# Optimization experiments

Measured on AMD Instinct MI355X. Metric: run time of the kernel, lower is better.

Reference implementation:

```python
import jax, jax.numpy as jnp
import numpy as np

BILATERAL = True
THETA_ALPHA = 8.0   # spatial bandwidth for bilateral term
THETA_BETA = 0.5    # color bandwidth for bilateral term
THETA_GAMMA = 3.0   # spatial bandwidth for spatial-only term


def _features(input_image):
    # input_image: [B, Ci, H, W] -> features [B, N, D]
    B, Ci, H, W = input_image.shape
    N = H * W
    ys, xs = jnp.meshgrid(jnp.arange(H, dtype=jnp.float32),
                          jnp.arange(W, dtype=jnp.float32), indexing='ij')
    pos = jnp.stack([ys, xs], axis=-1).reshape(N, 2)  # [N, 2]
    if BILATERAL:
        sp = jnp.broadcast_to(pos / THETA_ALPHA, (B, N, 2))
        col = input_image.reshape(B, Ci, N).transpose(0, 2, 1) / THETA_BETA  # [B, N, Ci]
        return jnp.concatenate([sp, col], axis=-1)  # [B, N, 2+Ci]
    else:
        return jnp.broadcast_to(pos / THETA_GAMMA, (B, N, 2))


def _gauss_filter(values, feats):
    # values: [B, C, N]; feats: [B, N, D] -> [B, C, N]
    # K_ij = exp(-0.5 * ||f_i - f_j||^2) (unnormalized, as in permutohedral filtering)
    sq = jnp.sum(feats * feats, axis=-1)  # [B, N]
    # squared distances: [B, N, N]
    d2 = sq[:, :, None] + sq[:, None, :] - 2.0 * jnp.einsum('bnd,bmd->bnm', feats, feats)
    K = jnp.exp(-0.5 * jnp.maximum(d2, 0.0))
    return jnp.einsum('bnm,bcm->bcn', K, values)


def setup_inputs() -> dict:
    key = jax.random.key(0)
    k1, k2 = jax.random.split(key)
    cur_state = jax.random.normal(k1, (2, 21, 96, 96), dtype=jnp.float32)
    input_image = jax.random.uniform(k2, (2, 3, 96, 96), dtype=jnp.float32)
    return {"cur_state": cur_state, "input_image": input_image}


def reference(cur_state, input_image):
    assert cur_state.ndim == 4
    B, C, H, W = cur_state.shape
    N = H * W
    feats = _features(input_image)                 # [B, N, D]
    vals = cur_state.reshape(B, C, N)              # [B, C, N]
    out = _gauss_filter(vals, feats)               # [B, C, N]
    return out.reshape(B, C, H, W)
```

## Files before the change

### kernel.cpp

```cpp
#include <hip/hip_runtime.h>
#include <hip/hip_bf16.h>
#include <math.h>


#define HH 96
#define WW 96
#define NN (HH * WW)
#define NB 2
#define NC 21

typedef __attribute__((ext_vector_type(8))) short short8;
typedef __attribute__((ext_vector_type(16))) float f32x16;
typedef __attribute__((ext_vector_type(2))) float float2v;

constexpr float INV_TA = 0.125f;
constexpr float INV_TB = 2.0f;
constexpr float LOG2E  = 1.44269504088896340736f;

constexpr int BLK    = 256;
constexpr int ITILE  = 64;
constexpr int NIT    = NN / ITILE;
constexpr int G      = 12;
constexpr int NPIECE = 36;
constexpr int NP     = NPIECE / G;

constexpr size_t VG_BYTES = (size_t)NB * NPIECE * 1024 * 16;
constexpr size_t FJA_OFF  = VG_BYTES;

constexpr int SMEM_BYTES = 4 * 32 * 33 * 4;

constexpr int NVU  = NB * NPIECE * 1024;
constexpr int NFT  = NB * NN;
constexpr int PREP_TASKS = NVU + NFT;

#if defined(__has_builtin)
#if __has_builtin(__builtin_amdgcn_exp2f)
#define EXP2F(x) __builtin_amdgcn_exp2f(x)
#endif
#if __has_builtin(__builtin_amdgcn_cvt_pk_bf16_f32)
#define HAS_CVT_PK_BF16 1
#endif
#endif
#ifndef EXP2F
#define EXP2F(x) exp2f(x)
#endif

__device__ __forceinline__ unsigned short bfh(float f) {
    return (unsigned short)((__float_as_uint(f) + 0x8000u) >> 16);
}
__device__ __forceinline__ float bff(unsigned short u) {
    return __uint_as_float(((unsigned)u) << 16);
}
__device__ __forceinline__ unsigned pack2bf(float a, float b) {
#ifdef HAS_CVT_PK_BF16
    auto t = __builtin_amdgcn_cvt_pk_bf16_f32(a, b);
    unsigned r; __builtin_memcpy(&r, &t, 4); return r;
#else
    const unsigned u0 = __float_as_uint(a) + 0x8000u;
    const unsigned u1 = __float_as_uint(b) + 0x8000u;
    return __builtin_amdgcn_perm(u1, u0, 0x07060302u);
#endif
}

__global__ __launch_bounds__(BLK)
void prep_kernel(const float* __restrict__ cur, const float* __restrict__ img,
                 unsigned char* __restrict__ ws) {
    const int t = blockIdx.x * BLK + threadIdx.x;
    if (t < NVU) {
        const int b  = t / (NPIECE * 1024);
        const int r  = t % (NPIECE * 1024);
        const int rr = r & 1023;
        const int piece = r >> 10;
        const int jbl = rr >> 7;
        const int m   = (rr >> 6) & 1;
        const int h   = (rr >> 5) & 1;
        const int c   = rr & 31;
        const int jb = piece * 256 + jbl * 32 + m * 16 + 4 * h;
        float4 qa = {0, 0, 0, 0}, qb = {0, 0, 0, 0};
        if (c < NC) {
            const float* row = cur + ((size_t)b * NC + c) * NN;
            qa = *(const float4*)(row + jb);
            qb = *(const float4*)(row + jb + 8);
        }
        uint4 o;
        o.x = pack2bf(qa.x, qa.y); o.y = pack2bf(qa.z, qa.w);
        o.z = pack2bf(qb.x, qb.y); o.w = pack2bf(qb.z, qb.w);
        *(uint4*)(ws + (size_t)t * 16) = o;
    } else {
        const int tf = t - NVU;
        const int b = tf / NN;
        const int j = tf % NN;
        const float y = (float)(j / WW) * INV_TA;
        const float x = (float)(j % WW) * INV_TA;
        const float* ib = img + (size_t)b * 3 * NN;
        unsigned short ch[3], cl[3]; float cf[3];
        #pragma unroll
        for (int d = 0; d < 3; ++d) {
            const float c = ib[d * NN + j] * INV_TB;
            ch[d] = bfh(c);
            const float chf = bff(ch[d]);
            cl[d] = bfh(c - chf);
            cf[d] = chf + bff(cl[d]);
        }
        const float e = -0.5f * (y * y + x * x +
                                 cf[0] * cf[0] + cf[1] * cf[1] + cf[2] * cf[2]);
        const unsigned short eh = bfh(e);
        const unsigned short el = bfh(e - bff(eh));
        const unsigned short one = 0x3F80;
        const int piece = j >> 8, jl = j & 255;
        unsigned short* u0 = (unsigned short*)
            (ws + FJA_OFF + ((((size_t)b * NPIECE + piece) * 2 + 0) * 256 + jl) * 16);
        unsigned short* u1 = (unsigned short*)
            (ws + FJA_OFF + ((((size_t)b * NPIECE + piece) * 2 + 1) * 256 + jl) * 16);
        u0[0] = bfh(y); u0[1] = bfh(x);
        u0[2] = ch[0]; u0[3] = ch[1]; u0[4] = ch[2];
        u0[5] = cl[0]; u0[6] = cl[1]; u0[7] = cl[2];
        u1[0] = ch[0]; u1[1] = ch[1]; u1[2] = ch[2]; u1[3] = eh; u1[4] = el;
        u1[5] = one; u1[6] = one; u1[7] = 0;
    }
}

__global__ __launch_bounds__(BLK)
void perm_gauss_mfma(const float* __restrict__ img,
                     const unsigned char* __restrict__ ws,
                     float* __restrict__ out) {
    __shared__ __align__(16) unsigned char smem[SMEM_BYTES];
    uint4* vlds = (uint4*)smem;

    const int tid  = threadIdx.x;
    const int lane = tid & 63;
    const int wave = tid >> 6;
    const int isub = wave & 1;
    const int jh   = wave >> 1;
    const int il   = lane & 31;
    const int half = lane >> 5;

    const int it = blockIdx.x, g = blockIdx.y, b = blockIdx.z;
    const int ibase = it * ITILE;
    const float* imgb = img + (size_t)b * 3 * NN;
    float* outb = out + (size_t)b * NC * NN;
    const unsigned short one = 0x3F80;

    const int ig = ibase + isub * 32 + il;
    const float yi = (float)(ig / WW) * INV_TA;
    const float xi = (float)(ig % WW) * INV_TA;
    unsigned short chi[3], cli[3]; float cfi[3];
    #pragma unroll
    for (int d = 0; d < 3; ++d) {
        const float c = imgb[d * NN + ig] * INV_TB;
        chi[d] = bfh(c);
        const float chf = bff(chi[d]);
        cli[d] = bfh(c - chf);
        cfi[d] = chf + bff(cli[d]);
    }
    const float ei = -0.5f * (yi * yi + xi * xi +
                              cfi[0] * cfi[0] + cfi[1] * cfi[1] + cfi[2] * cfi[2]);
    const unsigned short eih = bfh(ei);
    const unsigned short eil = bfh(ei - bff(eih));
    union { unsigned short u[8]; short8 v; } bfi;
    if (half == 0) {
        bfi.u[0] = bfh(yi); bfi.u[1] = bfh(xi);
        bfi.u[2] = chi[0]; bfi.u[3] = chi[1]; bfi.u[4] = chi[2];
        bfi.u[5] = chi[0]; bfi.u[6] = chi[1]; bfi.u[7] = chi[2];
    } else {
        bfi.u[0] = cli[0]; bfi.u[1] = cli[1]; bfi.u[2] = cli[2];
        bfi.u[3] = one; bfi.u[4] = one; bfi.u[5] = eih; bfi.u[6] = eil;
        bfi.u[7] = 0;
    }

    f32x16 acc0, acc1, zz;
    #pragma unroll
    for (int r = 0; r < 16; ++r) { acc0[r] = 0.0f; acc1[r] = 0.0f; zz[r] = 0.0f; }

    const float2v lg2 = {LOG2E, LOG2E};

    for (int p = 0; p < NP; ++p) {
        const int pidx = g * NP + p;
        __syncthreads();
        const uint4* vsrc = (const uint4*)(ws + ((size_t)b * NPIECE + pidx) * 16384);
        #pragma unroll
        for (int k = 0; k < 4; ++k) vlds[k * 256 + tid] = vsrc[k * 256 + tid];
        __syncthreads();

        const uint4* fws = (const uint4*)
            (ws + FJA_OFF + ((size_t)b * NPIECE + pidx) * 8192);

        #pragma unroll
        for (int q = 0; q < 4; ++q) {
            const int jbl = jh * 4 + q;
            short8 afj;
            { uint4 t = fws[half * 256 + jbl * 32 + il];
              __builtin_memcpy(&afj, &t, 16); }
            const f32x16 s =
                __builtin_amdgcn_mfma_f32_32x32x16_bf16(afj, bfi.v, zz, 0, 0, 0);
            union { f32x16 v; float2v p[8]; } su; su.v = s;
            float w[16];
            #pragma unroll
            for (int d8 = 0; d8 < 8; ++d8) {
                const float2v a = su.p[d8] * lg2;
                w[2 * d8]     = EXP2F(a.x);
                w[2 * d8 + 1] = EXP2F(a.y);
            }
            union { unsigned dw[4]; short8 v; } a1, a2;
            #pragma unroll
            for (int d = 0; d < 4; ++d) {
                a1.dw[d] = pack2bf(w[2 * d],     w[2 * d + 1]);
                a2.dw[d] = pack2bf(w[8 + 2 * d], w[9 + 2 * d]);
            }
            const short8 v1 = *(const short8*)&vlds[(4 * jbl + half) * 32 + il];
            const short8 v2 = *(const short8*)&vlds[(4 * jbl + 2 + half) * 32 + il];
            f32x16& A = (q & 1) ? acc1 : acc0;
            A = __builtin_amdgcn_mfma_f32_32x32x16_bf16(a1.v, v1, A, 0, 0, 0);
            A = __builtin_amdgcn_mfma_f32_32x32x16_bf16(a2.v, v2, A, 0, 0, 0);
        }
    }
    #pragma unroll
    for (int r = 0; r < 16; ++r) acc0[r] += acc1[r];

    __syncthreads();
    float* mytile = (float*)smem + wave * 32 * 33;
    #pragma unroll
    for (int r = 0; r < 16; ++r) {
        const int row = (r & 3) + 8 * (r >> 2) + 4 * half;
        mytile[row * 33 + il] = acc0[r];
    }
    #pragma unroll
    for (int cc = 0; cc < 11; ++cc) {
        const int c = 2 * cc + half;
        if (c < NC) {
            const float v = mytile[il * 33 + c];
            atomicAdd(&outb[(size_t)c * NN + ibase + isub * 32 + il], v);
        }
    }
}

extern "C" void kernel_launch(void* const* d_in, const int* in_sizes, int n_in,
                              void* d_out, int out_size, void* d_ws, size_t ws_size,
                              hipStream_t stream) {
    const float* cur = (const float*)d_in[0];
    const float* img = (const float*)d_in[1];
    float* out = (float*)d_out;
    unsigned char* ws = (unsigned char*)d_ws;

    prep_kernel<<<PREP_TASKS / BLK, BLK, 0, stream>>>(cur, img, ws);
    dim3 grid(NIT, G, NB);
    perm_gauss_mfma<<<grid, BLK, 0, stream>>>(img, ws, out);
}
```

Measured before the change: 98.12 us.

## Give each wave its own i-rows and preload all j pieces once per block

```diff
diff --git a/kernel.cpp b/kernel.cpp
--- a/kernel.cpp
+++ b/kernel.cpp
@@ -18,16 +18,16 @@
 constexpr float LOG2E  = 1.44269504088896340736f;
 
 constexpr int BLK    = 256;
-constexpr int ITILE  = 64;
+constexpr int ITILE  = 128;
 constexpr int NIT    = NN / ITILE;
-constexpr int G      = 12;
+constexpr int G      = 18;
+constexpr int NPP    = 2;
 constexpr int NPIECE = 36;
-constexpr int NP     = NPIECE / G;
 
 constexpr size_t VG_BYTES = (size_t)NB * NPIECE * 1024 * 16;
 constexpr size_t FJA_OFF  = VG_BYTES;
 
-constexpr int SMEM_BYTES = 4 * 32 * 33 * 4;
+constexpr int SMEM_BYTES = NPP * 1024 * 16;
 
 constexpr int NVU  = NB * NPIECE * 1024;
 constexpr int NFT  = NB * NN;
@@ -130,8 +130,6 @@
     const int tid  = threadIdx.x;
     const int lane = tid & 63;
     const int wave = tid >> 6;
-    const int isub = wave & 1;
-    const int jh   = wave >> 1;
     const int il   = lane & 31;
     const int half = lane >> 5;
 
@@ -141,7 +139,7 @@
     float* outb = out + (size_t)b * NC * NN;
     const unsigned short one = 0x3F80;
 
-    const int ig = ibase + isub * 32 + il;
+    const int ig = ibase + wave * 32 + il;
     const float yi = (float)(ig / WW) * INV_TA;
     const float xi = (float)(ig % WW) * INV_TA;
     unsigned short chi[3], cli[3]; float cfi[3];
@@ -168,28 +166,26 @@
         bfi.u[7] = 0;
     }
 
-    f32x16 acc0, acc1, zz;
-    #pragma unroll
-    for (int r = 0; r < 16; ++r) { acc0[r] = 0.0f; acc1[r] = 0.0f; zz[r] = 0.0f; }
-
+    const uint4* vsrc = (const uint4*)
+        (ws + ((size_t)b * NPIECE + (size_t)g * NPP) * 16384);
+    #pragma unroll
+    for (int k = 0; k < 8; ++k) vlds[k * 256 + tid] = vsrc[k * 256 + tid];
+    __syncthreads();
+
+    f32x16 acc, zz;
+    #pragma unroll
+    for (int r = 0; r < 16; ++r) { acc[r] = 0.0f; zz[r] = 0.0f; }
     const float2v lg2 = {LOG2E, LOG2E};
 
-    for (int p = 0; p < NP; ++p) {
-        const int pidx = g * NP + p;
-        __syncthreads();
-        const uint4* vsrc = (const uint4*)(ws + ((size_t)b * NPIECE + pidx) * 16384);
+    #pragma unroll 1
+    for (int pp = 0; pp < NPP; ++pp) {
+        const uint4* fws = (const uint4*)
+            (ws + FJA_OFF + ((size_t)b * NPIECE + (size_t)g * NPP + pp) * 8192);
+        const uint4* vp = vlds + pp * 1024;
         #pragma unroll
-        for (int k = 0; k < 4; ++k) vlds[k * 256 + tid] = vsrc[k * 256 + tid];
-        __syncthreads();
-
-        const uint4* fws = (const uint4*)
-            (ws + FJA_OFF + ((size_t)b * NPIECE + pidx) * 8192);
-
-        #pragma unroll
-        for (int q = 0; q < 4; ++q) {
-            const int jbl = jh * 4 + q;
+        for (int q = 0; q < 8; ++q) {
             short8 afj;
-            { uint4 t = fws[half * 256 + jbl * 32 + il];
+            { uint4 t = fws[half * 256 + q * 32 + il];
               __builtin_memcpy(&afj, &t, 16); }
             const f32x16 s =
                 __builtin_amdgcn_mfma_f32_32x32x16_bf16(afj, bfi.v, zz, 0, 0, 0);
@@ -207,29 +203,26 @@
                 a1.dw[d] = pack2bf(w[2 * d],     w[2 * d + 1]);
                 a2.dw[d] = pack2bf(w[8 + 2 * d], w[9 + 2 * d]);
             }
-            const short8 v1 = *(const short8*)&vlds[(4 * jbl + half) * 32 + il];
-            const short8 v2 = *(const short8*)&vlds[(4 * jbl + 2 + half) * 32 + il];
-            f32x16& A = (q & 1) ? acc1 : acc0;
-            A = __builtin_amdgcn_mfma_f32_32x32x16_bf16(a1.v, v1, A, 0, 0, 0);
-            A = __builtin_amdgcn_mfma_f32_32x32x16_bf16(a2.v, v2, A, 0, 0, 0);
-        }
-    }
-    #pragma unroll
-    for (int r = 0; r < 16; ++r) acc0[r] += acc1[r];
+            const short8 v1 = *(const short8*)&vp[(4 * q + half) * 32 + il];
+            const short8 v2 = *(const short8*)&vp[(4 * q + 2 + half) * 32 + il];
+            acc = __builtin_amdgcn_mfma_f32_32x32x16_bf16(a1.v, v1, acc, 0, 0, 0);
+            acc = __builtin_amdgcn_mfma_f32_32x32x16_bf16(a2.v, v2, acc, 0, 0, 0);
+        }
+    }
 
     __syncthreads();
     float* mytile = (float*)smem + wave * 32 * 33;
     #pragma unroll
     for (int r = 0; r < 16; ++r) {
         const int row = (r & 3) + 8 * (r >> 2) + 4 * half;
-        mytile[row * 33 + il] = acc0[r];
+        mytile[row * 33 + il] = acc[r];
     }
     #pragma unroll
     for (int cc = 0; cc < 11; ++cc) {
         const int c = 2 * cc + half;
         if (c < NC) {
             const float v = mytile[il * 33 + c];
-            atomicAdd(&outb[(size_t)c * NN + ibase + isub * 32 + il], v);
+            atomicAdd(&outb[(size_t)c * NN + ibase + wave * 32 + il], v);
         }
     }
 }
```

Measured after the change: 98.26 us. Within noise of the previous version (+0.1%).
